# Performance work log

Measured on AMD Instinct MI355X. Metric: run time of the kernel, lower is better.

Reference implementation:

```python
import jax, jax.numpy as jnp
import numpy as np

FEATS = [(100, 100), (50, 50), (25, 25), (13, 13)]  # (W, H) per level
BS, NQ, D = 2, 10000, 256
NH, NL, NP, G = 8, 4, 4, 8
HD = D // NH


def grid_sample_bilinear(im, grid):
    """torch.nn.functional.grid_sample(mode='bilinear', padding_mode='zeros', align_corners=False).
    im: [N, C, H, W]; grid: [N, Hg, Wg, 2] in [-1, 1] (x, y). Returns [N, C, Hg, Wg]."""
    N, C, H, W = im.shape
    Hg, Wg = grid.shape[1], grid.shape[2]
    x = (grid[..., 0] + 1.0) * (W * 0.5) - 0.5
    y = (grid[..., 1] + 1.0) * (H * 0.5) - 0.5
    x0 = jnp.floor(x); y0 = jnp.floor(y)
    wx1 = x - x0; wx0 = 1.0 - wx1
    wy1 = y - y0; wy0 = 1.0 - wy1
    imf = im.reshape(N, C, H * W)

    def corner(xi, yi, w):
        inb = (xi >= 0) & (xi < W) & (yi >= 0) & (yi < H)
        xi_c = jnp.clip(xi, 0, W - 1).astype(jnp.int32)
        yi_c = jnp.clip(yi, 0, H - 1).astype(jnp.int32)
        idx = (yi_c * W + xi_c).reshape(N, 1, Hg * Wg)
        vals = jnp.take_along_axis(imf, idx, axis=2).reshape(N, C, Hg, Wg)
        return vals * (w * inb.astype(im.dtype))[:, None]

    out = (corner(x0, y0, wx0 * wy0) + corner(x0 + 1, y0, wx1 * wy0)
           + corner(x0, y0 + 1, wx0 * wy1) + corner(x0 + 1, y0 + 1, wx1 * wy1))
    return out


def setup_inputs() -> dict:
    key = jax.random.key(0)
    ks = jax.random.split(key, 7)
    nv = sum(w * h for (w, h) in FEATS)
    return {
        "query": jax.random.normal(ks[0], (BS, NQ, D), jnp.float32),
        "value": jax.random.normal(ks[1], (BS, nv, NH, HD), jnp.float32),
        "reference_points": jax.random.uniform(ks[2], (BS, NQ, NL, 2), jnp.float32),
        "spatial_shapes": jnp.array(FEATS, jnp.float32),  # rows are (W, H)
        "W_off": jax.random.normal(ks[3], (NH * NL * NP * 2, D), jnp.float32) * 0.02,
        "b_off": jax.random.normal(ks[4], (NH * NL * NP * 2,), jnp.float32) * 0.5,
        "W_attn": jax.random.normal(ks[5], (NH * NL * NP, D), jnp.float32) * 0.02,
        "b_attn": jax.random.normal(ks[6], (NH * NL * NP,), jnp.float32) * 0.02,
    }


def reference(query, value, reference_points, spatial_shapes, W_off, b_off, W_attn, b_attn):
    bs, nq, _ = query.shape
    # sampling offsets: [bs, nq, NH, NL*NP*2] with (level, point, xy) layout
    off = (jnp.einsum('bqd,od->bqo', query, W_off) + b_off).reshape(bs, nq, NH, NL * NP * 2)
    # reference points tiled to the same (level, point, xy) layout
    ref = jnp.broadcast_to(reference_points[:, :, None, :, None, :],
                           (bs, nq, NH, NL, NP, 2)).reshape(bs, nq, NH, NL * NP * 2)
    # offset normalizer: (1/W, 1/H) per level, tiled over points
    inv = 1.0 / spatial_shapes  # [NL, 2]
    norm = jnp.broadcast_to(inv[:, None, :], (NL, NP, 2)).reshape(-1)
    loc = (ref + off * norm) * 2.0 - 1.0  # [bs, nq, NH, NL*NP*2]
    loc = loc.reshape(bs, nq, NH, NL, NP, 2)

    # attention weights: softmax over (NL*NP), then rearranged to [bs*NH, 1, nq/G, NL*G*NP]
    aw = jax.nn.softmax((jnp.einsum('bqd,od->bqo', query, W_attn) + b_attn)
                        .reshape(bs, nq, NH, NL * NP), axis=-1)
    aw = aw.reshape(bs, nq // G, G, NH, NL, NP).transpose(0, 3, 1, 4, 2, 5)
    aw = aw.reshape(bs * NH, 1, nq // G, NL * G * NP)

    # per-level grid_sample
    sizes = [w * h for (w, h) in FEATS]
    starts = np.concatenate([[0], np.cumsum(sizes)]).tolist()
    sampled = []
    for lvl, (Wl, Hl) in enumerate(FEATS):
        val_l = value[:, starts[lvl]:starts[lvl + 1]]  # [bs, Hl*Wl, NH, HD]
        val_l = val_l.transpose(0, 2, 3, 1).reshape(bs * NH, HD, Hl, Wl)
        grid_l = loc[:, :, :, lvl].transpose(0, 2, 1, 3, 4)  # [bs, NH, nq, NP, 2]
        grid_l = grid_l.reshape(bs * NH, nq // G, G * NP, 2)
        sampled.append(grid_sample_bilinear(val_l, grid_l))  # [bs*NH, HD, nq/G, G*NP]
    sv = jnp.concatenate(sampled, axis=-1)  # [bs*NH, HD, nq/G, NL*G*NP]

    out = sv * aw
    # reduce_sum linear (fixed 0/1 weight from init_weights) == sum over levels and points per group slot
    out = out.reshape(bs * NH, HD, nq // G, NL, G, NP).sum(axis=(3, 5))  # [bs*NH, HD, nq/G, G]
    return out.reshape(bs, NH * HD, nq)
```

## Files before the change

### kernel.cpp

```cpp
#include <hip/hip_runtime.h>

#define NQ   10000
#define BSZ  2
#define DIM  256
#define NH   8
#define HD   32
#define NLV  4
#define NPT  4
#define NV   13294
#define MT   (BSZ*NQ)
#define NOUT 384
#define NVAL (BSZ*NV*NH*HD)

typedef float  floatx4 __attribute__((ext_vector_type(4)));
typedef int    intx4   __attribute__((ext_vector_type(4)));
typedef __bf16 bf16x8  __attribute__((ext_vector_type(8)));

__device__ __forceinline__ unsigned short f32_to_bf16(float f) {
  unsigned int u = __float_as_uint(f);
  u += 0x7FFFu + ((u >> 16) & 1u);
  return (unsigned short)(u >> 16);
}

__global__ __launch_bounds__(256) void prep_kernel(
    const float* __restrict__ value, unsigned short* __restrict__ vb16) {
  int i = blockIdx.x * 256 + threadIdx.x;
  if (i * 4 < NVAL) {
    floatx4 v = *(const floatx4*)&value[i * 4];
    unsigned short t[4] = { f32_to_bf16(v.x), f32_to_bf16(v.y),
                            f32_to_bf16(v.z), f32_to_bf16(v.w) };
    *(uint2*)&vb16[i * 4] = *(const uint2*)t;
  }
}

__global__ __launch_bounds__(256) void gemm_kernel(
    const float* __restrict__ query, const float* __restrict__ W_off,
    const float* __restrict__ W_attn,
    const float* __restrict__ b_off, const float* __restrict__ b_attn,
    float* __restrict__ raw) {
  __shared__ unsigned short As[64][40];
  __shared__ unsigned short Bs[128][40];
  const int n0 = blockIdx.x * 128;
  const int m0 = blockIdx.y * 64;
  const int tid  = threadIdx.x;
  const int wave = tid >> 6;
  const int lane = tid & 63;
  const int quad = lane >> 4;
  const int l16  = lane & 15;
  floatx4 acc[8] = {};
  const int ar = tid >> 2;
  const int ac = (tid & 3) * 8;
  const int br = tid >> 1;
  const int bc = (tid & 1) * 16;
  const float* __restrict__ Wsrc =
      (n0 < 256) ? (W_off + (size_t)n0 * DIM) : (W_attn + (size_t)(n0 - 256) * DIM);

  for (int k0 = 0; k0 < DIM; k0 += 32) {
    {
      int gm = m0 + ar;
      floatx4 a0 = {}, a1 = {};
      if (gm < MT) {
        const float* src = query + (size_t)gm * DIM + k0 + ac;
        a0 = *(const floatx4*)src;
        a1 = *(const floatx4*)(src + 4);
      }
      unsigned short t[8];
      t[0]=f32_to_bf16(a0.x); t[1]=f32_to_bf16(a0.y); t[2]=f32_to_bf16(a0.z); t[3]=f32_to_bf16(a0.w);
      t[4]=f32_to_bf16(a1.x); t[5]=f32_to_bf16(a1.y); t[6]=f32_to_bf16(a1.z); t[7]=f32_to_bf16(a1.w);
      *(uint4*)&As[ar][ac] = *(const uint4*)t;
    }
    {
      const float* src = Wsrc + (size_t)br * DIM + k0 + bc;
      floatx4 b0 = *(const floatx4*)src;
      floatx4 b1 = *(const floatx4*)(src + 4);
      floatx4 b2 = *(const floatx4*)(src + 8);
      floatx4 b3 = *(const floatx4*)(src + 12);
      unsigned short t[16];
      t[0]=f32_to_bf16(b0.x);  t[1]=f32_to_bf16(b0.y);  t[2]=f32_to_bf16(b0.z);  t[3]=f32_to_bf16(b0.w);
      t[4]=f32_to_bf16(b1.x);  t[5]=f32_to_bf16(b1.y);  t[6]=f32_to_bf16(b1.z);  t[7]=f32_to_bf16(b1.w);
      t[8]=f32_to_bf16(b2.x);  t[9]=f32_to_bf16(b2.y);  t[10]=f32_to_bf16(b2.z); t[11]=f32_to_bf16(b2.w);
      t[12]=f32_to_bf16(b3.x); t[13]=f32_to_bf16(b3.y); t[14]=f32_to_bf16(b3.z); t[15]=f32_to_bf16(b3.w);
      *(uint4*)&Bs[br][bc]     = *(const uint4*)t;
      *(uint4*)&Bs[br][bc + 8] = *(const uint4*)(t + 8);
    }
    __syncthreads();
    bf16x8 a = *(const bf16x8*)&As[wave*16 + l16][quad*8];
    #pragma unroll
    for (int nt = 0; nt < 8; nt++) {
      bf16x8 b = *(const bf16x8*)&Bs[nt*16 + l16][quad*8];
      acc[nt] = __builtin_amdgcn_mfma_f32_16x16x32_bf16(a, b, acc[nt], 0, 0, 0);
    }
    __syncthreads();
  }
  #pragma unroll
  for (int nt = 0; nt < 8; nt++) {
    int gn = n0 + nt*16 + l16;
    float bias = (gn < 256) ? b_off[gn] : b_attn[gn - 256];
    #pragma unroll
    for (int r = 0; r < 4; r++) {
      int gm = m0 + wave*16 + quad*4 + r;
      if (gm < MT) raw[(size_t)gm*NOUT + gn] = acc[nt][r] + bias;
    }
  }
}

__global__ __launch_bounds__(256) void sample_kernel(
    const float* __restrict__ raw, const unsigned short* __restrict__ vb16,
    const float* __restrict__ refp, float* __restrict__ tmp) {
  const int b  = blockIdx.y;
  const int q0 = blockIdx.x * 4;
  const int mbase = b * NQ + q0;
  const int tid = threadIdx.x;

  __shared__ int   s_tab[4 * 8 * 132];
  __shared__ float s_aw[544];

  const int WLI[4] = {100, 50, 25, 13};
  const int STI[4] = {0, 10000, 12500, 13125};

  float rpx[2], rpy[2];

  #pragma unroll
  for (int it = 0; it < 2; ++it) {
    int slot = it * 256 + tid;
    int ql = slot >> 7, r = slot & 127, h = r >> 4, lp = r & 15, l = lp >> 2, p = lp & 3;
    int m = mbase + ql;
    const float* rp = raw + (size_t)m * NOUT;
    float offx = rp[h*32 + l*8 + p*2 + 0];
    float offy = rp[h*32 + l*8 + p*2 + 1];
    s_aw[(ql*8 + h)*17 + lp] = rp[256 + h*16 + lp];
    float Wl = (float)WLI[l];
    float rx = refp[(m*NLV + l)*2 + 0];
    float ry = refp[(m*NLV + l)*2 + 1];
    rpx[it] = rx * Wl + offx - 0.5f;
    rpy[it] = ry * Wl + offy - 0.5f;
  }
  __syncthreads();

  if (tid < 32) {
    int base = tid * 17;
    float mx = -1e30f;
    #pragma unroll
    for (int i = 0; i < 16; i++) mx = fmaxf(mx, s_aw[base + i]);
    float s = 0.f;
    float e[16];
    #pragma unroll
    for (int i = 0; i < 16; i++) { e[i] = expf(s_aw[base + i] - mx); s += e[i]; }
    float inv = 1.f / s;
    #pragma unroll
    for (int i = 0; i < 16; i++) s_aw[base + i] = e[i] * inv;
  }
  __syncthreads();

  #pragma unroll
  for (int it = 0; it < 2; ++it) {
    int slot = it * 256 + tid;
    int ql = slot >> 7, r = slot & 127, h = r >> 4, lp = r & 15, l = lp >> 2;
    float aw = s_aw[(ql*8 + h)*17 + lp];
    float px = rpx[it], py = rpy[it];
    float x0f = floorf(px), y0f = floorf(py);
    int x0 = (int)x0f, y0 = (int)y0f;
    float wx1 = px - x0f, wx0 = 1.f - wx1;
    float wy1 = py - y0f, wy0 = 1.f - wy1;
    int Wl = WLI[l], STl = STI[l];
    int row = (ql*8 + h) * 132 + lp * 8;
    #pragma unroll
    for (int t = 0; t < 4; ++t) {
      int xi = x0 + (t & 1), yi = y0 + (t >> 1);
      bool inb = (xi >= 0) & (xi < Wl) & (yi >= 0) & (yi < Wl);
      int off = inb ? ((STl + yi*Wl + xi) * 512 + h * 64) : 0;
      float w = inb ? (aw * ((t & 1) ? wx1 : wx0) * ((t >> 1) ? wy1 : wy0)) : 0.f;
      s_tab[row + t]     = off;
      s_tab[row + 4 + t] = __float_as_int(w);
    }
  }
  __syncthreads();

  const int ql = tid >> 6, lane = tid & 63, h = lane >> 3, cq = lane & 7;
  const char* vb = (const char*)vb16 + (size_t)b * (NV*NH*HD*2) + cq * 8;
  floatx4 acc = {0.f, 0.f, 0.f, 0.f};
  const int rbase = (ql*8 + h) * 132;
  #pragma unroll 4
  for (int pt = 0; pt < 16; ++pt) {
    intx4   offs = *(const intx4*)  &s_tab[rbase + pt*8];
    floatx4 ws   = *(const floatx4*)&s_tab[rbase + pt*8 + 4];
    uint2 u0 = *(const uint2*)(vb + offs.x);
    uint2 u1 = *(const uint2*)(vb + offs.y);
    uint2 u2 = *(const uint2*)(vb + offs.z);
    uint2 u3 = *(const uint2*)(vb + offs.w);
    #pragma unroll
    for (int t = 0; t < 4; ++t) {
      uint2 u = (t == 0) ? u0 : (t == 1) ? u1 : (t == 2) ? u2 : u3;
      float w = (t == 0) ? ws.x : (t == 1) ? ws.y : (t == 2) ? ws.z : ws.w;
      acc.x += w * __uint_as_float(u.x << 16);
      acc.y += w * __uint_as_float(u.x & 0xFFFF0000u);
      acc.z += w * __uint_as_float(u.y << 16);
      acc.w += w * __uint_as_float(u.y & 0xFFFF0000u);
    }
  }
  int m = mbase + ql;
  *(floatx4*)&tmp[(size_t)m * DIM + h*HD + cq*4] = acc;
}

__global__ __launch_bounds__(256) void transpose_kernel(
    const float* __restrict__ tmp, float* __restrict__ out) {
  __shared__ float tile[32][33];
  const int b  = blockIdx.z;
  const int q0 = blockIdx.x * 32;
  const int c0 = blockIdx.y * 32;
  const int tx = threadIdx.x & 31;
  const int ty = threadIdx.x >> 5;
  #pragma unroll
  for (int i = 0; i < 4; i++) {
    int qq = q0 + ty + i*8;
    tile[ty + i*8][tx] = (qq < NQ) ? tmp[((long)b*NQ + qq)*DIM + c0 + tx] : 0.f;
  }
  __syncthreads();
  if (q0 + tx < NQ) {
    #pragma unroll
    for (int i = 0; i < 4; i++) {
      out[((long)b*DIM + c0 + ty + i*8)*NQ + q0 + tx] = tile[tx][ty + i*8];
    }
  }
}

extern "C" void kernel_launch(void* const* d_in, const int* in_sizes, int n_in,
                              void* d_out, int out_size, void* d_ws, size_t ws_size,
                              hipStream_t stream) {
  const float* query  = (const float*)d_in[0];
  const float* value  = (const float*)d_in[1];
  const float* refp   = (const float*)d_in[2];
  const float* W_off  = (const float*)d_in[4];
  const float* b_off  = (const float*)d_in[5];
  const float* W_attn = (const float*)d_in[6];
  const float* b_attn = (const float*)d_in[7];
  float* out = (float*)d_out;

  char* ws = (char*)d_ws;
  float*          raw  = (float*)ws;
  float*          tmp  = (float*)(ws + 30720000);
  unsigned short* vb16 = (unsigned short*)(ws + 51200000);

  hipLaunchKernelGGL(prep_kernel, dim3((NVAL/4 + 255) / 256), dim3(256), 0, stream,
                     value, vb16);
  hipLaunchKernelGGL(gemm_kernel, dim3(3, 313), dim3(256), 0, stream,
                     query, W_off, W_attn, b_off, b_attn, raw);
  hipLaunchKernelGGL(sample_kernel, dim3(NQ / 4, BSZ), dim3(256), 0, stream,
                     raw, vb16, refp, tmp);
  hipLaunchKernelGGL(transpose_kernel, dim3(313, 8, 2), dim3(256), 0, stream,
                     tmp, out);
}
```

Measured before the change: 177.0 us.

## Merge prep and GEMM launches, widen sampler to 8 queries with 16B gathers

Folds the value-to-bf16 conversion into the projection GEMM launch as extra blocks, so one kernel launch and its inter-kernel gap go away. The sampling kernel now handles 8 queries per block and each lane gathers 8 channels (16-byte loads) instead of 4. Attention-times-bilinear weights are stored as bf16 in split shared-memory tables. This cuts per-block overhead and load instruction count, at the cost of lower weight precision and fewer blocks in flight per query batch.

```diff
diff --git a/kernel.cpp b/kernel.cpp
--- a/kernel.cpp
+++ b/kernel.cpp
@@ -11,6 +11,8 @@
 #define MT   (BSZ*NQ)
 #define NOUT 384
 #define NVAL (BSZ*NV*NH*HD)
+#define GEMM_BLOCKS 939
+#define PREP_BLOCKS 6647
 
 typedef float  floatx4 __attribute__((ext_vector_type(4)));
 typedef int    intx4   __attribute__((ext_vector_type(4)));
@@ -22,27 +24,28 @@
   return (unsigned short)(u >> 16);
 }
 
-__global__ __launch_bounds__(256) void prep_kernel(
-    const float* __restrict__ value, unsigned short* __restrict__ vb16) {
-  int i = blockIdx.x * 256 + threadIdx.x;
-  if (i * 4 < NVAL) {
-    floatx4 v = *(const floatx4*)&value[i * 4];
-    unsigned short t[4] = { f32_to_bf16(v.x), f32_to_bf16(v.y),
-                            f32_to_bf16(v.z), f32_to_bf16(v.w) };
-    *(uint2*)&vb16[i * 4] = *(const uint2*)t;
-  }
-}
-
-__global__ __launch_bounds__(256) void gemm_kernel(
+__global__ __launch_bounds__(256) void gp_kernel(
     const float* __restrict__ query, const float* __restrict__ W_off,
     const float* __restrict__ W_attn,
     const float* __restrict__ b_off, const float* __restrict__ b_attn,
-    float* __restrict__ raw) {
+    const float* __restrict__ value,
+    float* __restrict__ raw, unsigned short* __restrict__ vb16) {
+  const int bid = blockIdx.x;
+  const int tid = threadIdx.x;
+  if (bid >= GEMM_BLOCKS) {
+    int i = (bid - GEMM_BLOCKS) * 256 + tid;
+    if (i * 4 < NVAL) {
+      floatx4 v = *(const floatx4*)&value[i * 4];
+      unsigned short t[4] = { f32_to_bf16(v.x), f32_to_bf16(v.y),
+                              f32_to_bf16(v.z), f32_to_bf16(v.w) };
+      *(uint2*)&vb16[i * 4] = *(const uint2*)t;
+    }
+    return;
+  }
   __shared__ unsigned short As[64][40];
   __shared__ unsigned short Bs[128][40];
-  const int n0 = blockIdx.x * 128;
-  const int m0 = blockIdx.y * 64;
-  const int tid  = threadIdx.x;
+  const int n0 = (bid % 3) * 128;
+  const int m0 = (bid / 3) * 64;
   const int wave = tid >> 6;
   const int lane = tid & 63;
   const int quad = lane >> 4;
@@ -108,20 +111,21 @@
     const float* __restrict__ raw, const unsigned short* __restrict__ vb16,
     const float* __restrict__ refp, float* __restrict__ tmp) {
   const int b  = blockIdx.y;
-  const int q0 = blockIdx.x * 4;
+  const int q0 = blockIdx.x * 8;
   const int mbase = b * NQ + q0;
   const int tid = threadIdx.x;
 
-  __shared__ int   s_tab[4 * 8 * 132];
-  __shared__ float s_aw[544];
+  __shared__ int          s_off[64 * 68];
+  __shared__ unsigned int s_w  [64 * 34];
+  __shared__ float        s_aw [64 * 17];
 
   const int WLI[4] = {100, 50, 25, 13};
   const int STI[4] = {0, 10000, 12500, 13125};
 
-  float rpx[2], rpy[2];
-
-  #pragma unroll
-  for (int it = 0; it < 2; ++it) {
+  float rpx[4], rpy[4];
+
+  #pragma unroll
+  for (int it = 0; it < 4; ++it) {
     int slot = it * 256 + tid;
     int ql = slot >> 7, r = slot & 127, h = r >> 4, lp = r & 15, l = lp >> 2, p = lp & 3;
     int m = mbase + ql;
@@ -137,7 +141,7 @@
   }
   __syncthreads();
 
-  if (tid < 32) {
+  if (tid < 64) {
     int base = tid * 17;
     float mx = -1e30f;
     #pragma unroll
@@ -153,53 +157,69 @@
   __syncthreads();
 
   #pragma unroll
-  for (int it = 0; it < 2; ++it) {
+  for (int it = 0; it < 4; ++it) {
     int slot = it * 256 + tid;
     int ql = slot >> 7, r = slot & 127, h = r >> 4, lp = r & 15, l = lp >> 2;
-    float aw = s_aw[(ql*8 + h)*17 + lp];
+    int rowqh = ql*8 + h;
+    float aw = s_aw[rowqh*17 + lp];
     float px = rpx[it], py = rpy[it];
     float x0f = floorf(px), y0f = floorf(py);
     int x0 = (int)x0f, y0 = (int)y0f;
     float wx1 = px - x0f, wx0 = 1.f - wx1;
     float wy1 = py - y0f, wy0 = 1.f - wy1;
     int Wl = WLI[l], STl = STI[l];
-    int row = (ql*8 + h) * 132 + lp * 8;
+    int offs[4]; unsigned short wb[4];
     #pragma unroll
     for (int t = 0; t < 4; ++t) {
       int xi = x0 + (t & 1), yi = y0 + (t >> 1);
       bool inb = (xi >= 0) & (xi < Wl) & (yi >= 0) & (yi < Wl);
-      int off = inb ? ((STl + yi*Wl + xi) * 512 + h * 64) : 0;
+      offs[t] = inb ? ((STl + yi*Wl + xi) * 512 + h * 64) : 0;
       float w = inb ? (aw * ((t & 1) ? wx1 : wx0) * ((t >> 1) ? wy1 : wy0)) : 0.f;
-      s_tab[row + t]     = off;
-      s_tab[row + 4 + t] = __float_as_int(w);
-    }
-  }
-  __syncthreads();
-
-  const int ql = tid >> 6, lane = tid & 63, h = lane >> 3, cq = lane & 7;
-  const char* vb = (const char*)vb16 + (size_t)b * (NV*NH*HD*2) + cq * 8;
-  floatx4 acc = {0.f, 0.f, 0.f, 0.f};
-  const int rbase = (ql*8 + h) * 132;
+      wb[t] = f32_to_bf16(w);
+    }
+    *(intx4*)&s_off[rowqh*68 + lp*4] = *(const intx4*)offs;
+    uint2 wp = { (unsigned)wb[0] | ((unsigned)wb[1] << 16),
+                 (unsigned)wb[2] | ((unsigned)wb[3] << 16) };
+    *(uint2*)&s_w[rowqh*34 + lp*2] = wp;
+  }
+  __syncthreads();
+
+  const int wv = tid >> 6, lane = tid & 63;
+  const int qh = lane >> 5, ql = wv*2 + qh;
+  const int h = (lane >> 2) & 7, cq = lane & 3;
+  const char* vb = (const char*)vb16 + (size_t)b * (NV*NH*HD*2) + cq * 16;
+  floatx4 acc0 = {0.f,0.f,0.f,0.f}, acc1 = {0.f,0.f,0.f,0.f};
+  const int orow = (ql*8 + h) * 68, wrow = (ql*8 + h) * 34;
   #pragma unroll 4
   for (int pt = 0; pt < 16; ++pt) {
-    intx4   offs = *(const intx4*)  &s_tab[rbase + pt*8];
-    floatx4 ws   = *(const floatx4*)&s_tab[rbase + pt*8 + 4];
-    uint2 u0 = *(const uint2*)(vb + offs.x);
-    uint2 u1 = *(const uint2*)(vb + offs.y);
-    uint2 u2 = *(const uint2*)(vb + offs.z);
-    uint2 u3 = *(const uint2*)(vb + offs.w);
+    intx4 offs = *(const intx4*)&s_off[orow + pt*4];
+    uint2 wp   = *(const uint2*)&s_w[wrow + pt*2];
+    float w0 = __uint_as_float(wp.x << 16);
+    float w1 = __uint_as_float(wp.x & 0xFFFF0000u);
+    float w2 = __uint_as_float(wp.y << 16);
+    float w3 = __uint_as_float(wp.y & 0xFFFF0000u);
+    uint4 u0 = *(const uint4*)(vb + offs.x);
+    uint4 u1 = *(const uint4*)(vb + offs.y);
+    uint4 u2 = *(const uint4*)(vb + offs.z);
+    uint4 u3 = *(const uint4*)(vb + offs.w);
     #pragma unroll
     for (int t = 0; t < 4; ++t) {
-      uint2 u = (t == 0) ? u0 : (t == 1) ? u1 : (t == 2) ? u2 : u3;
-      float w = (t == 0) ? ws.x : (t == 1) ? ws.y : (t == 2) ? ws.z : ws.w;
-      acc.x += w * __uint_as_float(u.x << 16);
-      acc.y += w * __uint_as_float(u.x & 0xFFFF0000u);
-      acc.z += w * __uint_as_float(u.y << 16);
-      acc.w += w * __uint_as_float(u.y & 0xFFFF0000u);
+      uint4 u = (t==0) ? u0 : (t==1) ? u1 : (t==2) ? u2 : u3;
+      float w = (t==0) ? w0 : (t==1) ? w1 : (t==2) ? w2 : w3;
+      acc0.x += w * __uint_as_float(u.x << 16);
+      acc0.y += w * __uint_as_float(u.x & 0xFFFF0000u);
+      acc0.z += w * __uint_as_float(u.y << 16);
+      acc0.w += w * __uint_as_float(u.y & 0xFFFF0000u);
+      acc1.x += w * __uint_as_float(u.z << 16);
+      acc1.y += w * __uint_as_float(u.z & 0xFFFF0000u);
+      acc1.z += w * __uint_as_float(u.w << 16);
+      acc1.w += w * __uint_as_float(u.w & 0xFFFF0000u);
     }
   }
   int m = mbase + ql;
-  *(floatx4*)&tmp[(size_t)m * DIM + h*HD + cq*4] = acc;
+  float* dst = &tmp[(size_t)m * DIM + h*HD + cq*8];
+  *(floatx4*)dst       = acc0;
+  *(floatx4*)(dst + 4) = acc1;
 }
 
 __global__ __launch_bounds__(256) void transpose_kernel(
@@ -241,11 +261,9 @@
   float*          tmp  = (float*)(ws + 30720000);
   unsigned short* vb16 = (unsigned short*)(ws + 51200000);
 
-  hipLaunchKernelGGL(prep_kernel, dim3((NVAL/4 + 255) / 256), dim3(256), 0, stream,
-                     value, vb16);
-  hipLaunchKernelGGL(gemm_kernel, dim3(3, 313), dim3(256), 0, stream,
-                     query, W_off, W_attn, b_off, b_attn, raw);
-  hipLaunchKernelGGL(sample_kernel, dim3(NQ / 4, BSZ), dim3(256), 0, stream,
+  hipLaunchKernelGGL(gp_kernel, dim3(GEMM_BLOCKS + PREP_BLOCKS), dim3(256), 0, stream,
+                     query, W_off, W_attn, b_off, b_attn, value, raw, vb16);
+  hipLaunchKernelGGL(sample_kernel, dim3(NQ / 8, BSZ), dim3(256), 0, stream,
                      raw, vb16, refp, tmp);
   hipLaunchKernelGGL(transpose_kernel, dim3(313, 8, 2), dim3(256), 0, stream,
                      tmp, out);
```

New measurement: 169.0 us. -4.5%, faster.
